# Kernel tuning notes

Hardware: AMD Instinct MI355X
Metric: run time of the kernel (lower is better)

## Reference

```python
import jax, jax.numpy as jnp
import numpy as np

B = 16384  # batch
D = 64     # input_size (number of causal nodes)
H = 64     # hidden_size of each per-node MLP


def setup_inputs() -> dict:
    key = jax.random.key(0)
    k1, k2, k3 = jax.random.split(key, 3)
    inputs = jax.random.normal(k1, (B, D), dtype=jnp.float32)
    adjacency = jnp.ones((D, D), dtype=jnp.float32)  # buffer initialized to ones
    # stacked per-node weights: net_i = Linear(D->H, no bias) -> ReLU -> Linear(H->1, no bias)
    W1 = jax.random.normal(k2, (D, H, D), dtype=jnp.float32) * (1.0 / np.sqrt(D))
    W2 = jax.random.normal(k3, (D, H), dtype=jnp.float32) * (1.0 / np.sqrt(H))
    return {"inputs": inputs, "adjacency": adjacency, "W1": W1, "W2": W2}


def reference(inputs, adjacency, W1, W2):
    # inputs: [B, D]; adjacency: [D, D]; W1: [D, H, D]; W2: [D, H]
    # Original: repeat inputs to [B, D, D], mask rows by adjacency, then for each
    # node i apply its tiny MLP to row i and concat the scalar outputs -> [B, D].
    masked = inputs[:, None, :] * adjacency[None, :, :]          # [B, D, D]
    h = jax.nn.relu(jnp.einsum('bid,ihd->bih', masked, W1))      # [B, D, H]
    out = jnp.einsum('bih,ih->bi', h, W2)                        # [B, D]
    return out
```

## Files before the change

kernel.cpp:

```cpp
#include <hip/hip_runtime.h>
#include <hip/hip_bf16.h>

constexpr int BN = 16384;
constexpr int DN = 64;
constexpr int HN = 64;

typedef __attribute__((ext_vector_type(8))) short short8;
typedef __attribute__((ext_vector_type(4))) float f32x4;
typedef __attribute__((ext_vector_type(2))) float f32x2;

__device__ __forceinline__ unsigned short f2bf(float f) {
    __hip_bfloat16 h = __float2bfloat16(f);
    return *reinterpret_cast<unsigned short*>(&h);
}

__device__ __forceinline__ short8 cvt8(float4 a, float4 b) {
    short8 r;
    r[0] = (short)f2bf(a.x); r[1] = (short)f2bf(a.y);
    r[2] = (short)f2bf(a.z); r[3] = (short)f2bf(a.w);
    r[4] = (short)f2bf(b.x); r[5] = (short)f2bf(b.y);
    r[6] = (short)f2bf(b.z); r[7] = (short)f2bf(b.w);
    return r;
}

__global__ __launch_bounds__(256, 3) void mlp_fused_kernel(
    const float* __restrict__ X,
    const float* __restrict__ adj,
    const float* __restrict__ W1,
    const float* __restrict__ W2,
    float* __restrict__ out)
{
    const int btile = blockIdx.x & 127;
    const int ng    = blockIdx.x >> 7;
    const int tid   = threadIdx.x;
    const int wave  = tid >> 6;
    const int lane  = tid & 63;
    const int row16 = lane & 15;
    const int quad  = lane >> 4;

    __shared__ unsigned short ldsW1[4 * HN * DN];
    __shared__ float ldsW2[4 * HN];

    const int b0 = btile * 128 + wave * 32;
    short8 xfrag[2][2];
#pragma unroll
    for (int kk = 0; kk < 2; ++kk)
#pragma unroll
        for (int nt = 0; nt < 2; ++nt) {
            const float* p = X + (size_t)(b0 + nt * 16 + row16) * DN + kk * 32 + quad * 8;
            float4 v0 = *reinterpret_cast<const float4*>(p);
            float4 v1 = *reinterpret_cast<const float4*>(p + 4);
            xfrag[kk][nt] = cvt8(v0, v1);
        }

    {
        const float4* w4 = reinterpret_cast<const float4*>(W1 + (size_t)ng * 4 * HN * DN);
        const float4* a4 = reinterpret_cast<const float4*>(adj + (size_t)ng * 4 * DN);
#pragma unroll
        for (int it = 0; it < 8; ++it) {
            int chunk = it * 256 + tid;
            int nl = chunk >> 9;
            int h  = (chunk >> 3) & 63;
            int c  = chunk & 7;
            float4 w0 = w4[chunk * 2];
            float4 w1v = w4[chunk * 2 + 1];
            float4 a0 = a4[nl * 16 + c * 2];
            float4 a1 = a4[nl * 16 + c * 2 + 1];
            float4 m0 = {w0.x * a0.x, w0.y * a0.y, w0.z * a0.z, w0.w * a0.w};
            float4 m1 = {w1v.x * a1.x, w1v.y * a1.y, w1v.z * a1.z, w1v.w * a1.w};
            int elem = nl * 4096 + h * 64 + ((c ^ (h & 7)) << 3);
            *reinterpret_cast<short8*>(&ldsW1[elem]) = cvt8(m0, m1);
        }
        ldsW2[tid] = W2[ng * 256 + tid];
    }
    __syncthreads();

    float res[2][4];

#pragma unroll
    for (int j = 0; j < 4; ++j) {
        short8 wfrag[2][4];
#pragma unroll
        for (int kk = 0; kk < 2; ++kk)
#pragma unroll
            for (int mt = 0; mt < 4; ++mt) {
                int h = mt * 16 + row16;
                int elem = j * 4096 + h * 64 + (((kk * 4 + quad) ^ (row16 & 7)) << 3);
                wfrag[kk][mt] = *reinterpret_cast<const short8*>(&ldsW1[elem]);
            }

        float4 w2v[4];
#pragma unroll
        for (int mt = 0; mt < 4; ++mt)
            w2v[mt] = *reinterpret_cast<const float4*>(&ldsW2[j * 64 + mt * 16 + quad * 4]);

        f32x4 acc[4][2];
#pragma unroll
        for (int mt = 0; mt < 4; ++mt)
#pragma unroll
            for (int nt = 0; nt < 2; ++nt)
                acc[mt][nt] = (f32x4){0.f, 0.f, 0.f, 0.f};

#pragma unroll
        for (int kk = 0; kk < 2; ++kk)
#pragma unroll
            for (int mt = 0; mt < 4; ++mt) {
                acc[mt][0] = __builtin_amdgcn_mfma_f32_16x16x32_bf16(wfrag[kk][mt], xfrag[kk][0], acc[mt][0], 0, 0, 0);
                acc[mt][1] = __builtin_amdgcn_mfma_f32_16x16x32_bf16(wfrag[kk][mt], xfrag[kk][1], acc[mt][1], 0, 0, 0);
            }

#pragma unroll
        for (int nt = 0; nt < 2; ++nt) {
            f32x2 s = (f32x2){0.f, 0.f};
#pragma unroll
            for (int mt = 0; mt < 4; ++mt) {
                f32x2 m01 = (f32x2){fmaxf(acc[mt][nt][0], 0.f), fmaxf(acc[mt][nt][1], 0.f)};
                f32x2 m23 = (f32x2){fmaxf(acc[mt][nt][2], 0.f), fmaxf(acc[mt][nt][3], 0.f)};
                s += m01 * (f32x2){w2v[mt].x, w2v[mt].y};
                s += m23 * (f32x2){w2v[mt].z, w2v[mt].w};
            }
            float r = s[0] + s[1];
            r += __shfl_xor(r, 16);
            r += __shfl_xor(r, 32);
            res[nt][j] = r;
        }
    }

    if (quad < 2) {
        float4 v = (quad == 0)
            ? make_float4(res[0][0], res[0][1], res[0][2], res[0][3])
            : make_float4(res[1][0], res[1][1], res[1][2], res[1][3]);
        *reinterpret_cast<float4*>(out + (size_t)(b0 + quad * 16 + row16) * DN + ng * 4) = v;
    }
}

extern "C" void kernel_launch(void* const* d_in, const int* in_sizes, int n_in,
                              void* d_out, int out_size, void* d_ws, size_t ws_size,
                              hipStream_t stream) {
    const float* X   = (const float*)d_in[0];
    const float* adj = (const float*)d_in[1];
    const float* W1  = (const float*)d_in[2];
    const float* W2  = (const float*)d_in[3];
    float* out = (float*)d_out;

    (void)d_ws; (void)ws_size;

    mlp_fused_kernel<<<128 * 16, 256, 0, stream>>>(X, adj, W1, W2, out);
}
```

Before: 77.49 us.

## Double batch tile per block and stage X through swizzled LDS

Each block now handles 256 batch rows instead of 128, halving the grid so each W1 node-group tile staged in LDS is reused across twice as many rows. X is loaded cooperatively with coalesced float4 reads, converted to bf16, and stored swizzled in LDS, then read back as MFMA fragments. Each wave computes 4 N-tiles, doubling accumulator registers, and occupancy bounds drop from 3 to 2 blocks. This trades fewer redundant W1 loads and conversions for more LDS (extra 32KB), higher register pressure, and fewer blocks to hide latency.

```diff
diff --git a/kernel.cpp b/kernel.cpp
--- a/kernel.cpp
+++ b/kernel.cpp
@@ -23,15 +23,15 @@
     return r;
 }
 
-__global__ __launch_bounds__(256, 3) void mlp_fused_kernel(
+__global__ __launch_bounds__(256, 2) void mlp_fused_kernel(
     const float* __restrict__ X,
     const float* __restrict__ adj,
     const float* __restrict__ W1,
     const float* __restrict__ W2,
     float* __restrict__ out)
 {
-    const int btile = blockIdx.x & 127;
-    const int ng    = blockIdx.x >> 7;
+    const int btile = blockIdx.x & 63;
+    const int ng    = blockIdx.x >> 6;
     const int tid   = threadIdx.x;
     const int wave  = tid >> 6;
     const int lane  = tid & 63;
@@ -39,19 +39,24 @@
     const int quad  = lane >> 4;
 
     __shared__ unsigned short ldsW1[4 * HN * DN];
+    __shared__ unsigned short ldsX[256 * DN];
     __shared__ float ldsW2[4 * HN];
 
-    const int b0 = btile * 128 + wave * 32;
-    short8 xfrag[2][2];
+    const int b0 = btile * 256;
+
+    {
+        const float4* x4 = reinterpret_cast<const float4*>(X + (size_t)b0 * DN);
 #pragma unroll
-    for (int kk = 0; kk < 2; ++kk)
-#pragma unroll
-        for (int nt = 0; nt < 2; ++nt) {
-            const float* p = X + (size_t)(b0 + nt * 16 + row16) * DN + kk * 32 + quad * 8;
-            float4 v0 = *reinterpret_cast<const float4*>(p);
-            float4 v1 = *reinterpret_cast<const float4*>(p + 4);
-            xfrag[kk][nt] = cvt8(v0, v1);
+        for (int it = 0; it < 8; ++it) {
+            int chunk = it * 256 + tid;
+            int row = chunk >> 3;
+            int c   = chunk & 7;
+            float4 v0 = x4[chunk * 2];
+            float4 v1 = x4[chunk * 2 + 1];
+            int elem = row * 64 + ((c ^ (row & 7)) << 3);
+            *reinterpret_cast<short8*>(&ldsX[elem]) = cvt8(v0, v1);
         }
+    }
 
     {
         const float4* w4 = reinterpret_cast<const float4*>(W1 + (size_t)ng * 4 * HN * DN);
@@ -75,7 +80,17 @@
     }
     __syncthreads();
 
-    float res[2][4];
+    short8 xfrag[2][4];
+#pragma unroll
+    for (int kk = 0; kk < 2; ++kk)
+#pragma unroll
+        for (int nt = 0; nt < 4; ++nt) {
+            int row_l = wave * 64 + nt * 16 + row16;
+            int elem = row_l * 64 + (((kk * 4 + quad) ^ (row16 & 7)) << 3);
+            xfrag[kk][nt] = *reinterpret_cast<const short8*>(&ldsX[elem]);
+        }
+
+    float res[4][4];
 
 #pragma unroll
     for (int j = 0; j < 4; ++j) {
@@ -94,23 +109,24 @@
         for (int mt = 0; mt < 4; ++mt)
             w2v[mt] = *reinterpret_cast<const float4*>(&ldsW2[j * 64 + mt * 16 + quad * 4]);
 
-        f32x4 acc[4][2];
+        f32x4 acc[4][4];
 #pragma unroll
         for (int mt = 0; mt < 4; ++mt)
 #pragma unroll
-            for (int nt = 0; nt < 2; ++nt)
+            for (int nt = 0; nt < 4; ++nt)
                 acc[mt][nt] = (f32x4){0.f, 0.f, 0.f, 0.f};
 
 #pragma unroll
         for (int kk = 0; kk < 2; ++kk)
 #pragma unroll
-            for (int mt = 0; mt < 4; ++mt) {
-                acc[mt][0] = __builtin_amdgcn_mfma_f32_16x16x32_bf16(wfrag[kk][mt], xfrag[kk][0], acc[mt][0], 0, 0, 0);
-                acc[mt][1] = __builtin_amdgcn_mfma_f32_16x16x32_bf16(wfrag[kk][mt], xfrag[kk][1], acc[mt][1], 0, 0, 0);
-            }
+            for (int mt = 0; mt < 4; ++mt)
+#pragma unroll
+                for (int nt = 0; nt < 4; ++nt)
+                    acc[mt][nt] = __builtin_amdgcn_mfma_f32_16x16x32_bf16(
+                        wfrag[kk][mt], xfrag[kk][nt], acc[mt][nt], 0, 0, 0);
 
 #pragma unroll
-        for (int nt = 0; nt < 2; ++nt) {
+        for (int nt = 0; nt < 4; ++nt) {
             f32x2 s = (f32x2){0.f, 0.f};
 #pragma unroll
             for (int mt = 0; mt < 4; ++mt) {
@@ -126,12 +142,13 @@
         }
     }
 
-    if (quad < 2) {
-        float4 v = (quad == 0)
-            ? make_float4(res[0][0], res[0][1], res[0][2], res[0][3])
-            : make_float4(res[1][0], res[1][1], res[1][2], res[1][3]);
-        *reinterpret_cast<float4*>(out + (size_t)(b0 + quad * 16 + row16) * DN + ng * 4) = v;
-    }
+    float4 v = make_float4(0.f, 0.f, 0.f, 0.f);
+#pragma unroll
+    for (int nt = 0; nt < 4; ++nt)
+        if (quad == nt)
+            v = make_float4(res[nt][0], res[nt][1], res[nt][2], res[nt][3]);
+    int row = b0 + wave * 64 + quad * 16 + row16;
+    *reinterpret_cast<float4*>(out + (size_t)row * DN + ng * 4) = v;
 }
 
 extern "C" void kernel_launch(void* const* d_in, const int* in_sizes, int n_in,
@@ -145,5 +162,5 @@
 
     (void)d_ws; (void)ws_size;
 
-    mlp_fused_kernel<<<128 * 16, 256, 0, stream>>>(X, adj, W1, W2, out);
+    mlp_fused_kernel<<<64 * 16, 256, 0, stream>>>(X, adj, W1, W2, out);
 }
```

After: 75.88 us. -2.1%, faster.
